# Performance work log

Hardware: AMD Instinct MI355X
Metric: run time of the kernel (lower is better)

The kernel has to match this reference:

```python
import jax, jax.numpy as jnp
import numpy as np
from jax import lax

NEG_SLOPE = 0.01  # torch LeakyReLU default
PAD = 2           # (5-1)//2


def _depthwise_conv1d(x, w, b):
    # x: [B, C, L], w: [C, 1, K] (one filter per channel), b: [C]
    C = x.shape[1]
    y = lax.conv_general_dilated(
        x, w,
        window_strides=(1,),
        padding=[(PAD, PAD)],
        dimension_numbers=("NCH", "OIH", "NCH"),
        feature_group_count=C,
    )
    return y + b[None, :, None]


def setup_inputs() -> dict:
    key = jax.random.key(0)
    k1, k2, k3, k4, k5 = jax.random.split(key, 5)
    B, C, L, K = 128, 20, 10000, 5
    # fan_in for Conv1d(1,1,5) is 5 -> torch init bound = 1/sqrt(5)
    bound = 1.0 / np.sqrt(K)
    x = jax.random.normal(k1, (B, C, L), dtype=jnp.float32)
    w1 = jax.random.uniform(k2, (C, 1, K), jnp.float32, -bound, bound)
    b1 = jax.random.uniform(k3, (C,), jnp.float32, -bound, bound)
    w2 = jax.random.uniform(k4, (C, 1, K), jnp.float32, -bound, bound)
    b2 = jax.random.uniform(k5, (C,), jnp.float32, -bound, bound)
    return {"x": x, "w1": w1, "b1": b1, "w2": w2, "b2": b2}


def reference(x, w1, b1, w2, b2):
    # Equivalent to the per-channel Python loop: each channel c runs
    # conv1d(1->1) -> LeakyReLU -> conv1d(1->1) -> sigmoid, then gates x.
    h = _depthwise_conv1d(x, w1, b1)
    h = jnp.where(h >= 0, h, NEG_SLOPE * h)
    att = jax.nn.sigmoid(_depthwise_conv1d(h, w2, b2))
    return x * att
```

## Files before the change

### kernel.cpp

```cpp
#include <hip/hip_runtime.h>
#include <math.h>

#define BLOCK 256
#define VEC   4
#define TILE  (BLOCK * VEC)
#define KW    5
#define TPB   5

typedef float f32x4 __attribute__((ext_vector_type(4)));

__device__ __forceinline__ void load_tile(const float* __restrict__ xr,
                                          int i, int L, float a[12]) {
    if (i >= 4 && i + 7 < L) {
        f32x4 v0 = *reinterpret_cast<const f32x4*>(xr + i - 4);
        f32x4 v1 = *reinterpret_cast<const f32x4*>(xr + i);
        f32x4 v2 = *reinterpret_cast<const f32x4*>(xr + i + 4);
        #pragma unroll
        for (int e = 0; e < 4; ++e) {
            a[e] = v0[e]; a[4 + e] = v1[e]; a[8 + e] = v2[e];
        }
    } else {
        #pragma unroll
        for (int e = 0; e < 12; ++e) {
            int g = i - 4 + e;
            a[e] = (g >= 0 && g < L) ? xr[g] : 0.f;
        }
    }
}

__device__ __forceinline__ void compute_store(const float a[12], int i, int L,
                                              const float* W1, float B1,
                                              const float* W2, float B2,
                                              float* __restrict__ outr) {
    float h[8];
    #pragma unroll
    for (int j = 0; j < 8; ++j) {
        int p = i + j - 2;
        float acc = B1;
        #pragma unroll
        for (int k = 0; k < KW; ++k)
            acc = fmaf(W1[k], a[j + k], acc);
        acc = (acc >= 0.f) ? acc : 0.01f * acc;
        h[j] = (p >= 0 && p < L) ? acc : 0.f;
    }
    float res[4];
    #pragma unroll
    for (int e = 0; e < 4; ++e) {
        float z = B2;
        #pragma unroll
        for (int k = 0; k < KW; ++k)
            z = fmaf(W2[k], h[e + k], z);
        float s = __builtin_amdgcn_rcpf(1.f + __expf(-z));
        res[e] = a[4 + e] * s;
    }
    if (i + 3 < L) {
        f32x4 r = { res[0], res[1], res[2], res[3] };
        *reinterpret_cast<f32x4*>(outr + i) = r;
    } else {
        #pragma unroll
        for (int e = 0; e < 4; ++e)
            if (i + e < L) outr[i + e] = res[e];
    }
}

__global__ __launch_bounds__(BLOCK) void wav_attn_kernel(
    const float* __restrict__ x,
    const float* __restrict__ w1,
    const float* __restrict__ b1,
    const float* __restrict__ w2,
    const float* __restrict__ b2,
    float* __restrict__ out,
    int C, int L)
{
    const int row = blockIdx.y;
    const int c   = row % C;
    const float* xr   = x   + (long long)row * L;
    float*       outr = out + (long long)row * L;

    float W1[KW], W2[KW];
    #pragma unroll
    for (int k = 0; k < KW; ++k) {
        W1[k] = w1[c * KW + k];
        W2[k] = w2[c * KW + k];
    }
    const float B1 = b1[c];
    const float B2 = b2[c];

    int i = (blockIdx.x * TPB) * TILE + threadIdx.x * VEC;

    float aCur[12], aNxt[12] = {};
    load_tile(xr, i, L, aCur);

    #pragma unroll
    for (int t = 0; t < TPB; ++t) {
        const int iN = i + TILE;
        if (t + 1 < TPB)
            load_tile(xr, iN, L, aNxt);
        if (i < L)
            compute_store(aCur, i, L, W1, B1, W2, B2, outr);
        #pragma unroll
        for (int e = 0; e < 12; ++e) aCur[e] = aNxt[e];
        i = iN;
    }
}

extern "C" void kernel_launch(void* const* d_in, const int* in_sizes, int n_in,
                              void* d_out, int out_size, void* d_ws, size_t ws_size,
                              hipStream_t stream) {
    const float* x  = (const float*)d_in[0];
    const float* w1 = (const float*)d_in[1];
    const float* b1 = (const float*)d_in[2];
    const float* w2 = (const float*)d_in[3];
    const float* b2 = (const float*)d_in[4];
    float* out = (float*)d_out;

    const int C = in_sizes[2];
    const int B = 128;
    const int L = in_sizes[0] / (B * C);

    const int nTiles = (L + TILE - 1) / TILE;
    dim3 grid((nTiles + TPB - 1) / TPB, B * C);
    wav_attn_kernel<<<grid, BLOCK, 0, stream>>>(x, w1, b1, w2, b2, out, C, L);
}
```

Before: 191.3 us.

## Use one tile per block and add a branch-free interior fast path

```diff
diff --git a/kernel.cpp b/kernel.cpp
--- a/kernel.cpp
+++ b/kernel.cpp
@@ -5,63 +5,8 @@
 #define VEC   4
 #define TILE  (BLOCK * VEC)
 #define KW    5
-#define TPB   5
 
 typedef float f32x4 __attribute__((ext_vector_type(4)));
-
-__device__ __forceinline__ void load_tile(const float* __restrict__ xr,
-                                          int i, int L, float a[12]) {
-    if (i >= 4 && i + 7 < L) {
-        f32x4 v0 = *reinterpret_cast<const f32x4*>(xr + i - 4);
-        f32x4 v1 = *reinterpret_cast<const f32x4*>(xr + i);
-        f32x4 v2 = *reinterpret_cast<const f32x4*>(xr + i + 4);
-        #pragma unroll
-        for (int e = 0; e < 4; ++e) {
-            a[e] = v0[e]; a[4 + e] = v1[e]; a[8 + e] = v2[e];
-        }
-    } else {
-        #pragma unroll
-        for (int e = 0; e < 12; ++e) {
-            int g = i - 4 + e;
-            a[e] = (g >= 0 && g < L) ? xr[g] : 0.f;
-        }
-    }
-}
-
-__device__ __forceinline__ void compute_store(const float a[12], int i, int L,
-                                              const float* W1, float B1,
-                                              const float* W2, float B2,
-                                              float* __restrict__ outr) {
-    float h[8];
-    #pragma unroll
-    for (int j = 0; j < 8; ++j) {
-        int p = i + j - 2;
-        float acc = B1;
-        #pragma unroll
-        for (int k = 0; k < KW; ++k)
-            acc = fmaf(W1[k], a[j + k], acc);
-        acc = (acc >= 0.f) ? acc : 0.01f * acc;
-        h[j] = (p >= 0 && p < L) ? acc : 0.f;
-    }
-    float res[4];
-    #pragma unroll
-    for (int e = 0; e < 4; ++e) {
-        float z = B2;
-        #pragma unroll
-        for (int k = 0; k < KW; ++k)
-            z = fmaf(W2[k], h[e + k], z);
-        float s = __builtin_amdgcn_rcpf(1.f + __expf(-z));
-        res[e] = a[4 + e] * s;
-    }
-    if (i + 3 < L) {
-        f32x4 r = { res[0], res[1], res[2], res[3] };
-        *reinterpret_cast<f32x4*>(outr + i) = r;
-    } else {
-        #pragma unroll
-        for (int e = 0; e < 4; ++e)
-            if (i + e < L) outr[i + e] = res[e];
-    }
-}
 
 __global__ __launch_bounds__(BLOCK) void wav_attn_kernel(
     const float* __restrict__ x,
@@ -86,21 +31,91 @@
     const float B1 = b1[c];
     const float B2 = b2[c];
 
-    int i = (blockIdx.x * TPB) * TILE + threadIdx.x * VEC;
+    const int i = blockIdx.x * TILE + threadIdx.x * VEC;
+    const int lastBlk = gridDim.x - 1;
 
-    float aCur[12], aNxt[12] = {};
-    load_tile(xr, i, L, aCur);
+    if (blockIdx.x != 0 && blockIdx.x != lastBlk) {
+        f32x4 v0 = *reinterpret_cast<const f32x4*>(xr + i - 4);
+        f32x4 v1 = *reinterpret_cast<const f32x4*>(xr + i);
+        f32x4 v2 = *reinterpret_cast<const f32x4*>(xr + i + 4);
+        float a[12];
+        #pragma unroll
+        for (int e = 0; e < 4; ++e) {
+            a[e] = v0[e]; a[4 + e] = v1[e]; a[8 + e] = v2[e];
+        }
 
-    #pragma unroll
-    for (int t = 0; t < TPB; ++t) {
-        const int iN = i + TILE;
-        if (t + 1 < TPB)
-            load_tile(xr, iN, L, aNxt);
-        if (i < L)
-            compute_store(aCur, i, L, W1, B1, W2, B2, outr);
+        float h[8];
         #pragma unroll
-        for (int e = 0; e < 12; ++e) aCur[e] = aNxt[e];
-        i = iN;
+        for (int j = 0; j < 8; ++j) {
+            float acc = B1;
+            #pragma unroll
+            for (int k = 0; k < KW; ++k)
+                acc = fmaf(W1[k], a[j + k], acc);
+            h[j] = (acc >= 0.f) ? acc : 0.01f * acc;
+        }
+
+        float res[4];
+        #pragma unroll
+        for (int e = 0; e < 4; ++e) {
+            float z = B2;
+            #pragma unroll
+            for (int k = 0; k < KW; ++k)
+                z = fmaf(W2[k], h[e + k], z);
+            float s = __builtin_amdgcn_rcpf(1.f + __expf(-z));
+            res[e] = a[4 + e] * s;
+        }
+        f32x4 r = { res[0], res[1], res[2], res[3] };
+        *reinterpret_cast<f32x4*>(outr + i) = r;
+    } else {
+        if (i >= L) return;
+
+        float a[12];
+        if (i >= 4 && i + 7 < L) {
+            f32x4 v0 = *reinterpret_cast<const f32x4*>(xr + i - 4);
+            f32x4 v1 = *reinterpret_cast<const f32x4*>(xr + i);
+            f32x4 v2 = *reinterpret_cast<const f32x4*>(xr + i + 4);
+            #pragma unroll
+            for (int e = 0; e < 4; ++e) {
+                a[e] = v0[e]; a[4 + e] = v1[e]; a[8 + e] = v2[e];
+            }
+        } else {
+            #pragma unroll
+            for (int e = 0; e < 12; ++e) {
+                int g = i - 4 + e;
+                a[e] = (g >= 0 && g < L) ? xr[g] : 0.f;
+            }
+        }
+
+        float h[8];
+        #pragma unroll
+        for (int j = 0; j < 8; ++j) {
+            int p = i + j - 2;
+            float acc = B1;
+            #pragma unroll
+            for (int k = 0; k < KW; ++k)
+                acc = fmaf(W1[k], a[j + k], acc);
+            acc = (acc >= 0.f) ? acc : 0.01f * acc;
+            h[j] = (p >= 0 && p < L) ? acc : 0.f;
+        }
+
+        float res[4];
+        #pragma unroll
+        for (int e = 0; e < 4; ++e) {
+            float z = B2;
+            #pragma unroll
+            for (int k = 0; k < KW; ++k)
+                z = fmaf(W2[k], h[e + k], z);
+            float s = __builtin_amdgcn_rcpf(1.f + __expf(-z));
+            res[e] = a[4 + e] * s;
+        }
+        if (i + 3 < L) {
+            f32x4 r = { res[0], res[1], res[2], res[3] };
+            *reinterpret_cast<f32x4*>(outr + i) = r;
+        } else {
+            #pragma unroll
+            for (int e = 0; e < 4; ++e)
+                if (i + e < L) outr[i + e] = res[e];
+        }
     }
 }
 
@@ -118,7 +133,6 @@
     const int B = 128;
     const int L = in_sizes[0] / (B * C);
 
-    const int nTiles = (L + TILE - 1) / TILE;
-    dim3 grid((nTiles + TPB - 1) / TPB, B * C);
+    dim3 grid((L + TILE - 1) / TILE, B * C);
     wav_attn_kernel<<<grid, BLOCK, 0, stream>>>(x, w1, b1, w2, b2, out, C, L);
 }
```

After: 181.4 us. 5.2% less time.
